# Kernel optimization log

Measured on AMD Instinct MI355X. Metric: run time of the kernel, lower is better.

Reference implementation:

```python
import jax, jax.numpy as jnp
import numpy as np

D_MODEL = 1024
H = 16
D = D_MODEL // H  # 64 per-head dim
B, T = 2, 2048


def setup_inputs() -> dict:
    key = jax.random.key(0)
    ks = jax.random.split(key, 5)
    scale = 1.0 / np.sqrt(D_MODEL)
    x = jax.random.normal(ks[0], (B, T, D_MODEL), dtype=jnp.float32)
    Wqkv = jax.random.normal(ks[1], (D_MODEL, 3 * D_MODEL), dtype=jnp.float32) * scale
    bqkv = jnp.zeros((3 * D_MODEL,), dtype=jnp.float32)
    Wproj = jax.random.normal(ks[2], (D_MODEL, D_MODEL), dtype=jnp.float32) * scale
    bproj = jnp.zeros((D_MODEL,), dtype=jnp.float32)
    return {"x": x, "Wqkv": Wqkv, "bqkv": bqkv, "Wproj": Wproj, "bproj": bproj}


def reference(x, Wqkv, bqkv, Wproj, bproj):
    b, t, d_model = x.shape
    h, d = H, D
    qkv = x @ Wqkv + bqkv  # [b, t, 3*d_model]
    q, k, v = jnp.split(qkv, 3, axis=-1)
    # [b, t, d_model] -> [b, h, t, d]
    q = q.reshape(b, t, h, d).transpose(0, 2, 1, 3)
    k = k.reshape(b, t, h, d).transpose(0, 2, 1, 3)
    v = v.reshape(b, t, h, d).transpose(0, 2, 1, 3)
    att = jnp.einsum('bhqd,bhkd->bhqk', q, k) / jnp.sqrt(jnp.float32(d))
    causal = jnp.tril(jnp.ones((t, t), dtype=bool))  # [t, t]
    att = jnp.where(causal[None, None, :, :], att, -jnp.inf)
    att = jax.nn.softmax(att, axis=-1)
    # dropout in eval mode -> identity (deterministic reference)
    out = jnp.einsum('bhqk,bhkd->bhqd', att, v)  # [b, h, t, d]
    out = out.transpose(0, 2, 1, 3).reshape(b, t, d_model)
    out = out @ Wproj + bproj
    return out
```

## Files before the change

kernel.cpp:

```cpp
#include <hip/hip_runtime.h>
#include <cstddef>

typedef __bf16 bf16x8 __attribute__((ext_vector_type(8)));
typedef __bf16 bf16x4 __attribute__((ext_vector_type(4)));
typedef float  f32x4  __attribute__((ext_vector_type(4)));
typedef short  s16x4  __attribute__((ext_vector_type(4)));

union UBpk { bf16x4 b; s16x4 s; };

__device__ __forceinline__ float bf2f(unsigned short s) {
    return __uint_as_float(((unsigned int)s) << 16);
}
__device__ __forceinline__ unsigned short f2bf(float x) {
    unsigned int u = __float_as_uint(x);
    unsigned int r = u + 0x7fffu + ((u >> 16) & 1u);
    return (unsigned short)(r >> 16);
}

__device__ __forceinline__ unsigned cvt_pk_bf16(float lo, float hi) {
    unsigned r;
    asm("v_cvt_pk_bf16_f32 %0, %1, %2" : "=v"(r) : "v"(lo), "v"(hi));
    return r;
}

__device__ __forceinline__ float fast_exp2(float x) {
#if __has_builtin(__builtin_amdgcn_exp2f)
    return __builtin_amdgcn_exp2f(x);
#else
    return __expf(x * 0.6931471805599453f);
#endif
}

__device__ __forceinline__ void mfma16(f32x4& c, s16x4 a, s16x4 b) {
    c = __builtin_amdgcn_mfma_f32_16x16x16bf16_1k(a, b, c, 0, 0, 0);
}

__device__ __forceinline__ void async_load16(const void* g, void* l) {
    __builtin_amdgcn_global_load_lds(
        (const __attribute__((address_space(1))) unsigned int*)g,
        (__attribute__((address_space(3))) unsigned int*)l,
        16, 0, 0);
}

__global__ __launch_bounds__(256) void prep_kernel(
    const void* __restrict__ x, const void* __restrict__ Wqkv,
    const void* __restrict__ Wproj,
    unsigned short* __restrict__ xb, unsigned short* __restrict__ WqkvT,
    unsigned short* __restrict__ WprojT, int* __restrict__ flagp)
{
    __shared__ unsigned short T[64][72];
    __shared__ int cnt;
    const int tid = threadIdx.x;
    const int bid = blockIdx.x;

    if (tid == 0) cnt = 0;
    __syncthreads();
    {
        unsigned short u = ((const unsigned short*)x)[tid << 1];
        int e = (u >> 7) & 0xFF;
        int wild = ((e >= 0x90) || (e >= 1 && e <= 0x48)) ? 1 : 0;
        unsigned long long ball = __ballot(wild);
        if ((tid & 63) == 0) atomicAdd(&cnt, (int)__popcll(ball));
    }
    __syncthreads();
    const bool f32 = (cnt > 64);
    if (bid == 0 && tid == 0) *flagp = f32 ? 1 : 0;

    if (bid < 2048) {
        const size_t off = ((size_t)bid * 256 + tid) * 8;
        if (f32) {
            const float* s = (const float*)x + off;
            float4 a = *(const float4*)s;
            float4 b = *(const float4*)(s + 4);
            uint4 o;
            o.x = (unsigned)f2bf(a.x) | ((unsigned)f2bf(a.y) << 16);
            o.y = (unsigned)f2bf(a.z) | ((unsigned)f2bf(a.w) << 16);
            o.z = (unsigned)f2bf(b.x) | ((unsigned)f2bf(b.y) << 16);
            o.w = (unsigned)f2bf(b.z) | ((unsigned)f2bf(b.w) << 16);
            *(uint4*)(xb + off) = o;
        } else {
            *(uint4*)(xb + off) = *(const uint4*)((const unsigned short*)x + off);
        }
        return;
    }

    const void* src; unsigned short* dst; int C, bx, by;
    if (bid < 2048 + 768) {
        const int t2 = bid - 2048;
        src = Wqkv; dst = WqkvT; C = 3072;
        bx = t2 % 48; by = t2 / 48;
    } else {
        const int t2 = bid - 2816;
        src = Wproj; dst = WprojT; C = 1024;
        bx = t2 % 16; by = t2 / 16;
    }
    const int R = 1024;
    const int c0 = bx * 64, r0 = by * 64;
    const int r  = tid >> 2, cl = (tid & 3) << 4;

    unsigned short v[16];
    if (f32) {
        const float* s = (const float*)src + (size_t)(r0 + r) * C + c0 + cl;
        #pragma unroll
        for (int q = 0; q < 4; ++q) {
            float4 a = *(const float4*)(s + q * 4);
            v[q * 4 + 0] = f2bf(a.x); v[q * 4 + 1] = f2bf(a.y);
            v[q * 4 + 2] = f2bf(a.z); v[q * 4 + 3] = f2bf(a.w);
        }
    } else {
        const unsigned short* s = (const unsigned short*)src + (size_t)(r0 + r) * C + c0 + cl;
        uint4 a = *(const uint4*)s;
        uint4 b = *(const uint4*)(s + 8);
        unsigned int w[8] = {a.x, a.y, a.z, a.w, b.x, b.y, b.z, b.w};
        #pragma unroll
        for (int q = 0; q < 8; ++q) {
            v[q * 2]     = (unsigned short)(w[q] & 0xffffu);
            v[q * 2 + 1] = (unsigned short)(w[q] >> 16);
        }
    }
    #pragma unroll
    for (int c = 0; c < 16; ++c) T[cl + c][r] = v[c];
    __syncthreads();

    const int c = tid >> 2, rl = (tid & 3) << 4;
    uint4 o0 = *(const uint4*)&T[c][rl];
    uint4 o1 = *(const uint4*)&T[c][rl + 8];
    unsigned short* dp = dst + (size_t)(c0 + c) * R + r0 + rl;
    *(uint4*)dp       = o0;
    *(uint4*)(dp + 8) = o1;
}

__device__ __forceinline__ void bt_mainloop(
    const unsigned short* __restrict__ A,
    const unsigned short* __restrict__ BT,
    int K, int m0, int n0,
    unsigned short* As, unsigned short* Bs,
    f32x4 (&acc)[4][4])
{
    const int tid  = threadIdx.x;
    const int wave = tid >> 6;
    const int lane = tid & 63;
    const int mrow = lane & 15;
    const int quad = lane >> 4;
    const int wr = wave >> 1, wc = wave & 1;
    const int srow = tid >> 2;
    const int scol = (tid & 3) << 3;

    const unsigned short* ga  = A  + (size_t)(m0 + srow) * K + scol;
    const unsigned short* ga2 = ga + (size_t)64 * K;
    const unsigned short* gb  = BT + (size_t)(n0 + srow) * K + scol;
    const unsigned short* gb2 = gb + (size_t)64 * K;
    unsigned short* lA  = As + wave * 512;
    unsigned short* lA2 = As + 2048 + wave * 512;
    unsigned short* lB  = Bs + wave * 512;
    unsigned short* lB2 = Bs + 2048 + wave * 512;

    for (int k0 = 0; k0 < K; k0 += 32) {
        async_load16(ga,  lA);
        async_load16(ga2, lA2);
        async_load16(gb,  lB);
        async_load16(gb2, lB2);
        ga += 32; ga2 += 32; gb += 32; gb2 += 32;
        __syncthreads();

        bf16x8 afr[4], bfr[4];
        #pragma unroll
        for (int mt = 0; mt < 4; ++mt)
            afr[mt] = *(const bf16x8*)(As + (wr * 64 + mt * 16 + mrow) * 32 + quad * 8);
        #pragma unroll
        for (int nt = 0; nt < 4; ++nt)
            bfr[nt] = *(const bf16x8*)(Bs + (wc * 64 + nt * 16 + mrow) * 32 + quad * 8);
        #pragma unroll
        for (int mt = 0; mt < 4; ++mt) {
            #pragma unroll
            for (int nt = 0; nt < 4; ++nt)
                acc[mt][nt] = __builtin_amdgcn_mfma_f32_16x16x32_bf16(
                    afr[mt], bfr[nt], acc[mt][nt], 0, 0, 0);
        }
        __syncthreads();
    }
}

__global__ __launch_bounds__(256) void gemm_qkv_bt(
    const int* __restrict__ flag,
    const unsigned short* __restrict__ A,
    const unsigned short* __restrict__ BT,
    const void* __restrict__ bias,
    unsigned short* __restrict__ Qb, unsigned short* __restrict__ Kb,
    unsigned short* __restrict__ VbT)
{
    __shared__ unsigned short As[128 * 32];
    __shared__ unsigned short Bs[128 * 32];
    const int m0 = blockIdx.y * 128, n0 = blockIdx.x * 128;

    f32x4 acc[4][4];
    #pragma unroll
    for (int mt = 0; mt < 4; ++mt)
        #pragma unroll
        for (int nt = 0; nt < 4; ++nt)
            { acc[mt][nt][0]=0.f; acc[mt][nt][1]=0.f; acc[mt][nt][2]=0.f; acc[mt][nt][3]=0.f; }

    bt_mainloop(A, BT, 1024, m0, n0, As, Bs, acc);

    const int tid  = threadIdx.x;
    const int wave = tid >> 6;
    const int lane = tid & 63;
    const int mrow = lane & 15;
    const int quad = lane >> 4;
    const int wr = wave >> 1, wc = wave & 1;
    const bool f32b = (*flag != 0);

    #pragma unroll
    for (int nt = 0; nt < 4; ++nt) {
        const int n = n0 + wc * 64 + nt * 16 + mrow;
        const float bv = f32b ? ((const float*)bias)[n]
                              : bf2f(((const unsigned short*)bias)[n]);
        const int sel = n >> 10;
        const int h   = (n & 1023) >> 6;
        const int d   = n & 63;
        const float sc = (sel == 0) ? 0.18033688f : 1.0f;
        #pragma unroll
        for (int mt = 0; mt < 4; ++mt) {
            #pragma unroll
            for (int r = 0; r < 4; ++r) {
                const int m  = m0 + wr * 64 + mt * 16 + quad * 4 + r;
                const int bb = m >> 11;
                const int t  = m & 2047;
                const unsigned short ov = f2bf((acc[mt][nt][r] + bv) * sc);
                const int bhh = bb * 16 + h;
                if (sel == 0)      Qb [(((size_t)bhh * 2048 + t) << 6) + d] = ov;
                else if (sel == 1) Kb [(((size_t)bhh * 2048 + t) << 6) + d] = ov;
                else               VbT[((((size_t)bhh << 6) + d) << 11) + t] = ov;
            }
        }
    }
}

__global__ __launch_bounds__(256) void gemm_proj_n64(
    const int* __restrict__ flag,
    const unsigned short* __restrict__ A,
    const unsigned short* __restrict__ BT,
    const void* __restrict__ bias, void* __restrict__ Out)
{
    __shared__ unsigned short As[128 * 32];
    __shared__ unsigned short Bs[64 * 32];
    const int K = 1024;
    const int m0 = blockIdx.y * 128, n0 = blockIdx.x * 64;

    const int tid  = threadIdx.x;
    const int wave = tid >> 6;
    const int lane = tid & 63;
    const int mrow = lane & 15;
    const int quad = lane >> 4;
    const int wr = wave >> 1, wc = wave & 1;
    const int srow = tid >> 2;
    const int scol = (tid & 3) << 3;

    f32x4 acc[4][2];
    #pragma unroll
    for (int mt = 0; mt < 4; ++mt)
        #pragma unroll
        for (int nt = 0; nt < 2; ++nt)
            { acc[mt][nt][0]=0.f; acc[mt][nt][1]=0.f; acc[mt][nt][2]=0.f; acc[mt][nt][3]=0.f; }

    const unsigned short* ga  = A  + (size_t)(m0 + srow) * K + scol;
    const unsigned short* ga2 = ga + (size_t)64 * K;
    const unsigned short* gb  = BT + (size_t)(n0 + srow) * K + scol;
    unsigned short* lA  = As + wave * 512;
    unsigned short* lA2 = As + 2048 + wave * 512;
    unsigned short* lB  = Bs + wave * 512;

    for (int k0 = 0; k0 < K; k0 += 32) {
        async_load16(ga,  lA);
        async_load16(ga2, lA2);
        async_load16(gb,  lB);
        ga += 32; ga2 += 32; gb += 32;
        __syncthreads();

        bf16x8 afr[4], bfr[2];
        #pragma unroll
        for (int mt = 0; mt < 4; ++mt)
            afr[mt] = *(const bf16x8*)(As + (wr * 64 + mt * 16 + mrow) * 32 + quad * 8);
        #pragma unroll
        for (int nt = 0; nt < 2; ++nt)
            bfr[nt] = *(const bf16x8*)(Bs + (wc * 32 + nt * 16 + mrow) * 32 + quad * 8);
        #pragma unroll
        for (int mt = 0; mt < 4; ++mt) {
            #pragma unroll
            for (int nt = 0; nt < 2; ++nt)
                acc[mt][nt] = __builtin_amdgcn_mfma_f32_16x16x32_bf16(
                    afr[mt], bfr[nt], acc[mt][nt], 0, 0, 0);
        }
        __syncthreads();
    }

    const bool f32b = (*flag != 0);
    #pragma unroll
    for (int nt = 0; nt < 2; ++nt) {
        const int n = n0 + wc * 32 + nt * 16 + mrow;
        const float bv = f32b ? ((const float*)bias)[n]
                              : bf2f(((const unsigned short*)bias)[n]);
        #pragma unroll
        for (int mt = 0; mt < 4; ++mt) {
            #pragma unroll
            for (int r = 0; r < 4; ++r) {
                const int m = m0 + wr * 64 + mt * 16 + quad * 4 + r;
                const float val = acc[mt][nt][r] + bv;
                if (f32b) ((float*)Out)[(size_t)m * 1024 + n] = val;
                else      ((unsigned short*)Out)[(size_t)m * 1024 + n] = f2bf(val);
            }
        }
    }
}

__global__ __launch_bounds__(256) void attn_kernel(
    const unsigned short* __restrict__ Qb,
    const unsigned short* __restrict__ Kb,
    const unsigned short* __restrict__ VbT,
    unsigned short* __restrict__ Attn)
{
    __shared__ unsigned short Ks2[2][2][64 * 32];
    __shared__ unsigned short Vs2[2][64 * 64];

    const int tid  = threadIdx.x;
    const int wave = tid >> 6;
    const int lane = tid & 63;
    const int mrow = lane & 15;
    const int quad = lane >> 4;

    const int blk  = blockIdx.x;
    const int xcd  = blk & 7;
    const int j    = blk >> 3;
    const int s    = j >> 5;
    const int w    = j & 31;
    const int t8   = w >> 2;
    const int bh   = (xcd << 2) | (w & 3);
    const int qblk = (s == 0) ? 31 - t8 : (s == 1) ? 23 - t8
                   : (s == 2) ? 8 + t8   : t8;
    const int q0   = qblk << 6;
    const int nr   = qblk + 1;
    const int b    = bh >> 4, h = bh & 15;

    const int lc    = tid & 63;
    const int sc_   = lc ^ ((lc >> 3) & 7);
    const int grow  = wave * 16 + (sc_ >> 2);
    const int gcol8 = (sc_ & 3) << 3;
    const int ldst  = tid * 8;

    const int vrow0 = tid >> 3;
    const int vcol  = (((tid & 7) ^ (vrow0 & 7)) << 3);

    const int swzro = ((mrow * 4 + quad) ^ ((mrow >> 1) & 7)) << 3;

    const int m7 = mrow & 7, qh = quad >> 1, ql = quad & 1;
    int voff[4];
    #pragma unroll
    for (int jt = 0; jt < 4; ++jt)
        voff[jt] = (((2 * jt + qh) ^ m7) << 3) + (ql << 2);

    const unsigned short* Qbase = Qb  + ((size_t)bh << 17);
    const unsigned short* Kbase = Kb  + ((size_t)bh << 17);
    const unsigned short* Vtb   = VbT + ((size_t)bh << 17);

    s16x4 ones4 = { 0x3F80, 0x3F80, 0x3F80, 0x3F80 };
    const float SHIFT = 23.083120654223414f;

    bf16x8 aq[2];
    {
        const unsigned short* qp = Qbase + (size_t)(q0 + wave * 16 + mrow) * 64 + quad * 8;
        aq[0] = *(const bf16x8*)qp;
        aq[1] = *(const bf16x8*)(qp + 32);
    }

    f32x4 Oa[4];
    #pragma unroll
    for (int dt = 0; dt < 4; ++dt) { Oa[dt][0]=0.f; Oa[dt][1]=0.f; Oa[dt][2]=0.f; Oa[dt][3]=0.f; }
    f32x4 la; la[0]=0.f; la[1]=0.f; la[2]=0.f; la[3]=0.f;

    #pragma unroll
    for (int h2 = 0; h2 < 2; ++h2)
        async_load16(Kbase + (size_t)grow * 64 + h2 * 32 + gcol8,
                     &Ks2[0][h2][ldst]);
    async_load16(Vtb + (size_t)vrow0 * 2048 + vcol, &Vs2[0][tid * 8]);
    async_load16(Vtb + (size_t)(vrow0 + 32) * 2048 + vcol, &Vs2[0][2048 + tid * 8]);

    for (int rr = 0; rr < nr; ++rr) {
        __syncthreads();

        if (rr + 1 < nr) {
            const int nt0 = (rr + 1) << 6;
            const int nb  = (rr + 1) & 1;
            #pragma unroll
            for (int h2 = 0; h2 < 2; ++h2)
                async_load16(Kbase + (size_t)(nt0 + grow) * 64 + h2 * 32 + gcol8,
                             &Ks2[nb][h2][ldst]);
            async_load16(Vtb + (size_t)vrow0 * 2048 + nt0 + vcol,
                         &Vs2[nb][tid * 8]);
            async_load16(Vtb + (size_t)(vrow0 + 32) * 2048 + nt0 + vcol,
                         &Vs2[nb][2048 + tid * 8]);
        }

        const int cb  = rr & 1;
        const int kt0 = rr << 6;

        f32x4 sacc[4];
        #pragma unroll
        for (int jt = 0; jt < 4; ++jt) { sacc[jt][0]=0.f; sacc[jt][1]=0.f; sacc[jt][2]=0.f; sacc[jt][3]=0.f; }
        #pragma unroll
        for (int ks = 0; ks < 2; ++ks) {
            #pragma unroll
            for (int jt = 0; jt < 4; ++jt) {
                bf16x8 bk = *(const bf16x8*)&Ks2[cb][ks][jt * 512 + swzro];
                sacc[jt] = __builtin_amdgcn_mfma_f32_16x16x32_bf16(bk, aq[ks], sacc[jt], 0, 0, 0);
            }
        }

        if (rr == nr - 1) {
            const int qg = q0 + wave * 16 + mrow;
            #pragma unroll
            for (int jt = 0; jt < 4; ++jt) {
                #pragma unroll
                for (int r = 0; r < 4; ++r) {
                    const int jg = kt0 + jt * 16 + quad * 4 + r;
                    if (jg > qg) sacc[jt][r] = -1e30f;
                }
            }
        }

        s16x4 up[4];
        #pragma unroll
        for (int jt = 0; jt < 4; ++jt) {
            UBpk uu;
            uu.b[0] = (__bf16)fast_exp2(sacc[jt][0] - SHIFT);
            uu.b[1] = (__bf16)fast_exp2(sacc[jt][1] - SHIFT);
            uu.b[2] = (__bf16)fast_exp2(sacc[jt][2] - SHIFT);
            uu.b[3] = (__bf16)fast_exp2(sacc[jt][3] - SHIFT);
            up[jt] = uu.s;
        }

        #pragma unroll
        for (int dt = 0; dt < 4; ++dt) {
            const int vb = (dt * 16 + mrow) << 6;
            #pragma unroll
            for (int jt = 0; jt < 4; ++jt) {
                s16x4 vf = *(const s16x4*)&Vs2[cb][vb + voff[jt]];
                mfma16(Oa[dt], vf, up[jt]);
            }
        }
        #pragma unroll
        for (int jt = 0; jt < 4; ++jt)
            mfma16(la, ones4, up[jt]);
    }

    const float inv = 1.0f / la[0];
    const int   qg  = q0 + wave * 16 + mrow;
    const size_t base = ((size_t)(b * 2048 + qg)) * 1024 + h * 64 + quad * 4;
    #pragma unroll
    for (int dt = 0; dt < 4; ++dt) {
        uint2 o;
        o.x = cvt_pk_bf16(Oa[dt][0] * inv, Oa[dt][1] * inv);
        o.y = cvt_pk_bf16(Oa[dt][2] * inv, Oa[dt][3] * inv);
        *(uint2*)(Attn + base + dt * 16) = o;
    }
}

extern "C" void kernel_launch(void* const* d_in, const int* in_sizes, int n_in,
                              void* d_out, int out_size, void* d_ws, size_t ws_size,
                              hipStream_t stream)
{
    const void* x     = d_in[0];
    const void* Wqkv  = d_in[1];
    const void* bqkv  = d_in[2];
    const void* Wproj = d_in[3];
    const void* bproj = d_in[4];

    int* flag = (int*)d_ws;
    unsigned short* ws = (unsigned short*)d_ws;
    unsigned short* xb     = ws + 64;
    unsigned short* shared = xb + 4194304;
    unsigned short* WqkvT  = shared;
    unsigned short* Attn   = shared;
    unsigned short* WprojT = shared + 4194304;
    unsigned short* Qb     = WprojT + 1048576;
    unsigned short* Kb     = Qb + 4194304;
    unsigned short* VbT    = Kb + 4194304;

    prep_kernel<<<3072, 256, 0, stream>>>(x, Wqkv, Wproj, xb, WqkvT, WprojT, flag);
    gemm_qkv_bt<<<dim3(24, 32), 256, 0, stream>>>(flag, xb, WqkvT, bqkv, Qb, Kb, VbT);
    attn_kernel<<<1024, 256, 0, stream>>>(Qb, Kb, VbT, Attn);
    gemm_proj_n64<<<dim3(16, 32), 256, 0, stream>>>(flag, Attn, WprojT, bproj, d_out);
}
```

Baseline: 187.7 us.

## Double-buffer LDS tiles in QKV GEMM with async prefetch two stages ahead

Inlines the GEMM mainloop into the QKV projection kernel and switches from a single LDS buffer to two. The next K-tile's global-to-LDS async loads are issued while the current tile is computed, using explicit vmcnt waits and raw s_barrier instead of __syncthreads. This aims to hide global load latency behind MFMA work, at the cost of doubled LDS use and fragile hand-managed wait counts.

Measured after the change: 189.1 us. About the same (+0.8%).

```diff
diff --git a/kernel.cpp b/kernel.cpp
--- a/kernel.cpp
+++ b/kernel.cpp
@@ -130,13 +130,19 @@
     *(uint4*)(dp + 8) = o1;
 }
 
-__device__ __forceinline__ void bt_mainloop(
+__global__ __launch_bounds__(256) void gemm_qkv_bt(
+    const int* __restrict__ flag,
     const unsigned short* __restrict__ A,
     const unsigned short* __restrict__ BT,
-    int K, int m0, int n0,
-    unsigned short* As, unsigned short* Bs,
-    f32x4 (&acc)[4][4])
+    const void* __restrict__ bias,
+    unsigned short* __restrict__ Qb, unsigned short* __restrict__ Kb,
+    unsigned short* __restrict__ VbT)
 {
+    __shared__ unsigned short As[2 * 4096];
+    __shared__ unsigned short Bs[2 * 4096];
+    const int K = 1024;
+    const int m0 = blockIdx.y * 128, n0 = blockIdx.x * 128;
+
     const int tid  = threadIdx.x;
     const int wave = tid >> 6;
     const int lane = tid & 63;
@@ -150,26 +156,41 @@
     const unsigned short* ga2 = ga + (size_t)64 * K;
     const unsigned short* gb  = BT + (size_t)(n0 + srow) * K + scol;
     const unsigned short* gb2 = gb + (size_t)64 * K;
-    unsigned short* lA  = As + wave * 512;
-    unsigned short* lA2 = As + 2048 + wave * 512;
-    unsigned short* lB  = Bs + wave * 512;
-    unsigned short* lB2 = Bs + 2048 + wave * 512;
-
-    for (int k0 = 0; k0 < K; k0 += 32) {
-        async_load16(ga,  lA);
-        async_load16(ga2, lA2);
-        async_load16(gb,  lB);
-        async_load16(gb2, lB2);
-        ga += 32; ga2 += 32; gb += 32; gb2 += 32;
-        __syncthreads();
-
+    const int lofs  = wave * 512;
+    const int lofs2 = 2048 + wave * 512;
+
+    f32x4 acc[4][4];
+    #pragma unroll
+    for (int mt = 0; mt < 4; ++mt)
+        #pragma unroll
+        for (int nt = 0; nt < 4; ++nt)
+            { acc[mt][nt][0]=0.f; acc[mt][nt][1]=0.f; acc[mt][nt][2]=0.f; acc[mt][nt][3]=0.f; }
+
+    async_load16(ga,       As + lofs);
+    async_load16(ga2,      As + lofs2);
+    async_load16(gb,       Bs + lofs);
+    async_load16(gb2,      Bs + lofs2);
+    async_load16(ga  + 32, As + 4096 + lofs);
+    async_load16(ga2 + 32, As + 4096 + lofs2);
+    async_load16(gb  + 32, Bs + 4096 + lofs);
+    async_load16(gb2 + 32, Bs + 4096 + lofs2);
+    ga += 64; ga2 += 64; gb += 64; gb2 += 64;
+
+    const int NT = K >> 5;
+    for (int t = 0; t < NT; ++t) {
+        if (t + 1 < NT) asm volatile("s_waitcnt vmcnt(4)" ::: "memory");
+        else            asm volatile("s_waitcnt vmcnt(0)" ::: "memory");
+        asm volatile("s_barrier" ::: "memory");
+
+        const unsigned short* Ac = As + (t & 1) * 4096;
+        const unsigned short* Bc = Bs + (t & 1) * 4096;
         bf16x8 afr[4], bfr[4];
         #pragma unroll
         for (int mt = 0; mt < 4; ++mt)
-            afr[mt] = *(const bf16x8*)(As + (wr * 64 + mt * 16 + mrow) * 32 + quad * 8);
+            afr[mt] = *(const bf16x8*)(Ac + (wr * 64 + mt * 16 + mrow) * 32 + quad * 8);
         #pragma unroll
         for (int nt = 0; nt < 4; ++nt)
-            bfr[nt] = *(const bf16x8*)(Bs + (wc * 64 + nt * 16 + mrow) * 32 + quad * 8);
+            bfr[nt] = *(const bf16x8*)(Bc + (wc * 64 + nt * 16 + mrow) * 32 + quad * 8);
         #pragma unroll
         for (int mt = 0; mt < 4; ++mt) {
             #pragma unroll
@@ -177,39 +198,20 @@
                 acc[mt][nt] = __builtin_amdgcn_mfma_f32_16x16x32_bf16(
                     afr[mt], bfr[nt], acc[mt][nt], 0, 0, 0);
         }
-        __syncthreads();
-    }
-}
-
-__global__ __launch_bounds__(256) void gemm_qkv_bt(
-    const int* __restrict__ flag,
-    const unsigned short* __restrict__ A,
-    const unsigned short* __restrict__ BT,
-    const void* __restrict__ bias,
-    unsigned short* __restrict__ Qb, unsigned short* __restrict__ Kb,
-    unsigned short* __restrict__ VbT)
-{
-    __shared__ unsigned short As[128 * 32];
-    __shared__ unsigned short Bs[128 * 32];
-    const int m0 = blockIdx.y * 128, n0 = blockIdx.x * 128;
-
-    f32x4 acc[4][4];
-    #pragma unroll
-    for (int mt = 0; mt < 4; ++mt)
-        #pragma unroll
-        for (int nt = 0; nt < 4; ++nt)
-            { acc[mt][nt][0]=0.f; acc[mt][nt][1]=0.f; acc[mt][nt][2]=0.f; acc[mt][nt][3]=0.f; }
-
-    bt_mainloop(A, BT, 1024, m0, n0, As, Bs, acc);
-
-    const int tid  = threadIdx.x;
-    const int wave = tid >> 6;
-    const int lane = tid & 63;
-    const int mrow = lane & 15;
-    const int quad = lane >> 4;
-    const int wr = wave >> 1, wc = wave & 1;
+
+        asm volatile("s_barrier" ::: "memory");
+        if (t + 2 < NT) {
+            unsigned short* Ad = As + (t & 1) * 4096;
+            unsigned short* Bd = Bs + (t & 1) * 4096;
+            async_load16(ga,  Ad + lofs);
+            async_load16(ga2, Ad + lofs2);
+            async_load16(gb,  Bd + lofs);
+            async_load16(gb2, Bd + lofs2);
+            ga += 32; ga2 += 32; gb += 32; gb2 += 32;
+        }
+    }
+
     const bool f32b = (*flag != 0);
-
     #pragma unroll
     for (int nt = 0; nt < 4; ++nt) {
         const int n = n0 + wc * 64 + nt * 16 + mrow;
```
